# Optimization experiments

Hardware: AMD Instinct MI355X
Metric: run time of the kernel (lower is better)

## Reference

```python
import jax, jax.numpy as jnp
import numpy as np

EMBED_DIM = 128
SEQ_LEN = 2048
NUM_PHENOTYPES = 1
NUM_LAYERS = 3
INIT_SCALE = 0.03
BATCH = 32


def setup_inputs() -> dict:
    key = jax.random.key(0)
    ks = jax.random.split(key, 10)
    genotypes = jax.random.normal(ks[0], (BATCH, SEQ_LEN), dtype=jnp.float32)
    emb = INIT_SCALE * jax.random.normal(ks[1], (SEQ_LEN, EMBED_DIM), dtype=jnp.float32)
    # torch Linear weights are (out, in); stacked over layers
    qw = INIT_SCALE * jax.random.normal(ks[2], (NUM_LAYERS, EMBED_DIM, EMBED_DIM), dtype=jnp.float32)
    kw = INIT_SCALE * jax.random.normal(ks[3], (NUM_LAYERS, EMBED_DIM, EMBED_DIM), dtype=jnp.float32)
    vw = INIT_SCALE * jax.random.normal(ks[4], (NUM_LAYERS, EMBED_DIM, EMBED_DIM), dtype=jnp.float32)
    qb = jnp.zeros((NUM_LAYERS, EMBED_DIM), dtype=jnp.float32)
    kb = jnp.zeros((NUM_LAYERS, EMBED_DIM), dtype=jnp.float32)
    vb = jnp.zeros((NUM_LAYERS, EMBED_DIM), dtype=jnp.float32)
    bound = 1.0 / np.sqrt(SEQ_LEN * EMBED_DIM)
    rw = jax.random.uniform(ks[5], (NUM_PHENOTYPES, SEQ_LEN * EMBED_DIM), dtype=jnp.float32, minval=-bound, maxval=bound)
    rb = jax.random.uniform(ks[6], (NUM_PHENOTYPES,), dtype=jnp.float32, minval=-bound, maxval=bound)
    return {"genotypes": genotypes, "emb": emb, "qw": qw, "qb": qb,
            "kw": kw, "kb": kb, "vw": vw, "vb": vb, "rw": rw, "rb": rb}


def reference(genotypes, emb, qw, qb, kw, kb, vw, vb, rw, rb):
    # x: (B, L, D) = genotype value scales locus embedding
    x = genotypes[:, :, None] * emb[None, :, :]
    for i in range(NUM_LAYERS):
        # torch Linear: y = x @ W.T + b
        q = jnp.einsum('bld,ed->ble', x, qw[i]) + qb[i]
        k = jnp.einsum('bld,ed->ble', x, kw[i]) + kb[i]
        v = jnp.einsum('bld,ed->ble', x, vw[i]) + vb[i]
        scores = jnp.einsum('bqd,bkd->bqk', q, k)  # (B, L, L), unscaled
        attn = jax.nn.softmax(scores, axis=-1)
        x = jnp.einsum('bqk,bkd->bqd', attn, v)  # no skip connections
    x_flat = x.reshape(x.shape[0], -1)  # (B, L*D)
    return x_flat @ rw.T + rb  # (B, num_phenotypes)
```

## Files before the change

kernel.cpp:

```cpp
#include <hip/hip_runtime.h>
#include <hip/hip_bf16.h>

#define B_   32
#define L_   2048
#define D_   128
#define NL_  3
#define KVB  64
#define NKT  (L_ / KVB)

typedef __attribute__((ext_vector_type(8))) short short8;
typedef __attribute__((ext_vector_type(4))) float f32x4;
typedef __attribute__((ext_vector_type(16))) float f32x16;

__device__ __forceinline__ short f2bf(float f) {
    unsigned u = __builtin_bit_cast(unsigned, f);
    u += 0x7fffu + ((u >> 16) & 1u);
    return (short)(u >> 16);
}
__device__ __forceinline__ unsigned pk2(float a, float b) {
    unsigned ua = __builtin_bit_cast(unsigned, a);
    ua += 0x7fffu + ((ua >> 16) & 1u);
    unsigned ub = __builtin_bit_cast(unsigned, b);
    ub += 0x7fffu + ((ub >> 16) & 1u);
    return (ua >> 16) | (ub & 0xffff0000u);
}
__device__ __forceinline__ void plswap(unsigned& a, unsigned& b) {
    asm volatile("v_permlane32_swap_b32 %0, %1" : "+v"(a), "+v"(b));
}

__device__ __forceinline__ void gll16(const void* g, void* l) {
    __builtin_amdgcn_global_load_lds(
        (__attribute__((address_space(1))) void*)(g),
        (__attribute__((address_space(3))) void*)(l), 16, 0, 0);
}


__global__ __launch_bounds__(256) void k_form_x(const float* __restrict__ g,
                                                const float* __restrict__ emb,
                                                short* __restrict__ X) {
    int tid = blockIdx.x * 256 + threadIdx.x;
    int bl  = tid >> 4;
    int d8  = (tid & 15) << 3;
    int l   = bl & (L_ - 1);
    float gv = g[bl];
    const float4* e = reinterpret_cast<const float4*>(emb + (size_t)l * D_ + d8);
    float4 a = e[0], b = e[1];
    short8 r;
    r[0]=f2bf(a.x*gv); r[1]=f2bf(a.y*gv); r[2]=f2bf(a.z*gv); r[3]=f2bf(a.w*gv);
    r[4]=f2bf(b.x*gv); r[5]=f2bf(b.y*gv); r[6]=f2bf(b.z*gv); r[7]=f2bf(b.w*gv);
    *reinterpret_cast<short8*>(X + (size_t)tid * 8) = r;
}

__global__ __launch_bounds__(256) void k_convw(const float* __restrict__ qw,
                                               const float* __restrict__ kw,
                                               const float* __restrict__ vw,
                                               short* __restrict__ Wbf) {
    const float* src = (blockIdx.y == 0) ? qw : (blockIdx.y == 1) ? kw : vw;
    int tid = blockIdx.x * 256 + threadIdx.x;
    int layer = tid >> 11;
    int i = tid & 2047;
    int Lb = i * 16;
    int row = Lb >> 8, c = (Lb & 255) ^ ((row & 7) << 4);
    const float4* p = reinterpret_cast<const float4*>(src + (size_t)layer * 16384 + row * 128 + (c >> 1));
    float4 a = p[0], b = p[1];
    short8 s;
    s[0]=f2bf(a.x); s[1]=f2bf(a.y); s[2]=f2bf(a.z); s[3]=f2bf(a.w);
    s[4]=f2bf(b.x); s[5]=f2bf(b.y); s[6]=f2bf(b.z); s[7]=f2bf(b.w);
    size_t off = ((size_t)layer * 3 + blockIdx.y) * 16384;
    *reinterpret_cast<short8*>(Wbf + off + (size_t)i * 8) = s;
}

__global__ __launch_bounds__(256, 2) void k_qkv(const short* __restrict__ X,
    const short* __restrict__ Wl,
    const float* __restrict__ bq, const float* __restrict__ bk, const float* __restrict__ bv,
    short* __restrict__ Qf, short* __restrict__ Kf, short* __restrict__ Vf) {
    __shared__ short xs[128 * 128];
    __shared__ short wsh[128 * 128];
    const int t = threadIdx.x;
    int flat = blockIdx.x, xcd = flat & 7, idx = flat >> 3;
    int mat = idx >> 6, rblk = xcd * 64 + (idx & 63);
    const float* bias = (mat == 0) ? bq : (mat == 1) ? bk : bv;
    const short* Wg = Wl + (size_t)mat * 16384;
    const size_t rowbase = (size_t)rblk * 128;

    const char* Xg = reinterpret_cast<const char*>(X) + rowbase * 256;
#pragma unroll
    for (int p = 0; p < 8; p++) {
        int Lb = (p * 256 + t) * 16;
        int row = Lb >> 8, c = Lb & 255;
        gll16(Xg + (size_t)row * 256 + (c ^ ((row & 7) << 4)),
              reinterpret_cast<char*>(xs) + Lb);
    }
#pragma unroll
    for (int p = 0; p < 8; p++) {
        int Lb = (p * 256 + t) * 16;
        gll16(reinterpret_cast<const char*>(Wg) + Lb,
              reinterpret_cast<char*>(wsh) + Lb);
    }
    __syncthreads();

    const int wave = t >> 6, lane = t & 63, g = lane >> 4, ln = lane & 15;
    const int bb2 = (int)(rowbase >> 11);
    const int l0  = (int)(rowbase & (L_ - 1));
    f32x4 acc[2][8];
#pragma unroll
    for (int mi = 0; mi < 2; mi++)
#pragma unroll
        for (int ni = 0; ni < 8; ni++) acc[mi][ni] = f32x4{0.f, 0.f, 0.f, 0.f};

    if (mat < 2) {
#pragma unroll
        for (int kk = 0; kk < 4; kk++) {
            short8 aW[2];
#pragma unroll
            for (int mi = 0; mi < 2; mi++) {
                int row = wave * 32 + mi * 16 + ln;
                int byte = (row * 256 + kk * 64 + g * 16) ^ ((row & 7) << 4);
                aW[mi] = *reinterpret_cast<const short8*>(reinterpret_cast<const char*>(wsh) + byte);
            }
#pragma unroll
            for (int ni = 0; ni < 8; ni++) {
                int row = ni * 16 + ln;
                int byte = (row * 256 + kk * 64 + g * 16) ^ ((row & 7) << 4);
                short8 bX = *reinterpret_cast<const short8*>(reinterpret_cast<const char*>(xs) + byte);
                acc[0][ni] = __builtin_amdgcn_mfma_f32_16x16x32_bf16(aW[0], bX, acc[0][ni], 0, 0, 0);
                acc[1][ni] = __builtin_amdgcn_mfma_f32_16x16x32_bf16(aW[1], bX, acc[1][ni], 0, 0, 0);
            }
        }
        char* oc = reinterpret_cast<char*>((mat == 0) ? Qf : Kf) + ((size_t)bb2 << 19);
        int lidx_hi = ((g >> 1) & 1) << 5;
#pragma unroll
        for (int mi = 0; mi < 2; mi++) {
            int e0 = wave * 32 + mi * 16 + g * 4;
            int dst = wave * 2 + mi;
            float4 b4 = *reinterpret_cast<const float4*>(bias + e0);
#pragma unroll
            for (int ni = 0; ni < 8; ni++) {
                unsigned lo = (unsigned short)f2bf(acc[mi][ni][0] + b4.x)
                            | ((unsigned)(unsigned short)f2bf(acc[mi][ni][1] + b4.y) << 16);
                unsigned hi2 = (unsigned short)f2bf(acc[mi][ni][2] + b4.z)
                            | ((unsigned)(unsigned short)f2bf(acc[mi][ni][3] + b4.w) << 16);
                int blk32 = (l0 >> 5) + (ni >> 1);
                int l31 = ((ni & 1) << 4) + ln;
                size_t off = ((size_t)(blk32 * 8 + dst) << 10)
                           + ((lidx_hi + l31) << 4) + ((g & 1) << 3);
                int2 pk; pk.x = (int)lo; pk.y = (int)hi2;
                *reinterpret_cast<int2*>(oc + off) = pk;
            }
        }
    } else {
#pragma unroll
        for (int kk = 0; kk < 4; kk++) {
            short8 aX[2];
#pragma unroll
            for (int mi = 0; mi < 2; mi++) {
                int row = wave * 32 + mi * 16 + ln;
                int byte = (row * 256 + kk * 64 + g * 16) ^ ((row & 7) << 4);
                aX[mi] = *reinterpret_cast<const short8*>(reinterpret_cast<const char*>(xs) + byte);
            }
#pragma unroll
            for (int ni = 0; ni < 8; ni++) {
                int row = ni * 16 + ln;
                int byte = (row * 256 + kk * 64 + g * 16) ^ ((row & 7) << 4);
                short8 bW = *reinterpret_cast<const short8*>(reinterpret_cast<const char*>(wsh) + byte);
                acc[0][ni] = __builtin_amdgcn_mfma_f32_16x16x32_bf16(aX[0], bW, acc[0][ni], 0, 0, 0);
                acc[1][ni] = __builtin_amdgcn_mfma_f32_16x16x32_bf16(aX[1], bW, acc[1][ni], 0, 0, 0);
            }
        }
        char* oc = reinterpret_cast<char*>(Vf) + ((size_t)bb2 << 19);
#pragma unroll
        for (int ni = 0; ni < 8; ni++) {
            int d = ni * 16 + ln;
            float bvv = bias[d];
            int d2 = d >> 5, d31 = d & 31;
#pragma unroll
            for (int mi = 0; mi < 2; mi++) {
                unsigned lo = (unsigned short)f2bf(acc[mi][ni][0] + bvv)
                            | ((unsigned)(unsigned short)f2bf(acc[mi][ni][1] + bvv) << 16);
                unsigned hi2 = (unsigned short)f2bf(acc[mi][ni][2] + bvv)
                            | ((unsigned)(unsigned short)f2bf(acc[mi][ni][3] + bvv) << 16);
                int lglob = l0 + wave * 32 + mi * 16 + g * 4;
                int kt = lglob >> 6, k16 = (lglob >> 4) & 3, lhi = (lglob >> 3) & 1;
                size_t off = ((size_t)kt << 14) + (k16 << 12) + (d2 << 10)
                           + ((lhi * 32 + d31) << 4) + ((g & 1) << 3);
                int2 pk; pk.x = (int)lo; pk.y = (int)hi2;
                *reinterpret_cast<int2*>(oc + off) = pk;
            }
        }
    }
}

__global__ __launch_bounds__(256, 3) void k_attn(const short* __restrict__ Qf,
                                                 const short* __restrict__ Kf,
                                                 const short* __restrict__ Vf,
                                                 short* __restrict__ Xo,
                                                 const float* __restrict__ rw,
                                                 const float* __restrict__ rb,
                                                 float* __restrict__ out,
                                                 int fuse) {
    __shared__ short Ks[2][KVB * 128];
    __shared__ short Vts[128 * KVB];
    const int t = threadIdx.x, w = t >> 6, lane = t & 63;
    const int hi = lane >> 5, c5 = lane & 31;
    int flat = blockIdx.x;
    int xcd = flat & 7, idx = flat >> 3;
    int b = xcd * 4 + (idx >> 4), qt = idx & 15;
    const size_t qbase = (size_t)b * L_ + qt * 128;

    const char* Qg = reinterpret_cast<const char*>(Qf) + ((size_t)b << 19);
    short8 qf[8];
#pragma unroll
    for (int dst = 0; dst < 8; dst++)
        qf[dst] = *reinterpret_cast<const short8*>(
            Qg + (((size_t)(qt * 4 + w) * 8 + dst) << 10) + lane * 16);
    __builtin_amdgcn_sched_barrier(0);

    const char* Kg = reinterpret_cast<const char*>(Kf) + ((size_t)b << 19);
    const char* Vg = reinterpret_cast<const char*>(Vf) + ((size_t)b << 19);

    auto stageK = [&](int kt, int buf) {
#pragma unroll
        for (int p = 0; p < 4; p++) {
            int Lb = (p * 256 + t) * 16;
            gll16(Kg + ((size_t)kt << 14) + Lb, reinterpret_cast<char*>(Ks[buf]) + Lb);
        }
    };
    auto stageV = [&](int kt) {
#pragma unroll
        for (int p = 0; p < 4; p++) {
            int Lb = (p * 256 + t) * 16;
            gll16(Vg + ((size_t)kt << 14) + Lb, reinterpret_cast<char*>(Vts) + Lb);
        }
    };

    stageK(0, 0);
    stageV(0);
    stageK(1, 1);

    f32x16 o[4];
#pragma unroll
    for (int d2 = 0; d2 < 4; d2++)
#pragma unroll
        for (int r = 0; r < 16; r++) o[d2][r] = 0.f;
    float lsum = 0.f;

    for (int kt = 0; kt < NKT; kt++) {
        if (kt < NKT - 1) asm volatile("s_waitcnt vmcnt(4)" ::: "memory");
        else              asm volatile("s_waitcnt vmcnt(0)" ::: "memory");
        __builtin_amdgcn_sched_barrier(0);
        __builtin_amdgcn_s_barrier();

        const char* Kb8 = reinterpret_cast<const char*>(Ks[kt & 1]) + lane * 16;
        const char* Vb8 = reinterpret_cast<const char*>(Vts) + lane * 16;

        f32x16 s0, s1;
#pragma unroll
        for (int r = 0; r < 16; r++) { s0[r] = 0.f; s1[r] = 0.f; }
        __builtin_amdgcn_s_setprio(1);
#pragma unroll
        for (int dst = 0; dst < 8; dst++) {
            short8 kf0 = *reinterpret_cast<const short8*>(Kb8 + dst * 1024);
            short8 kf1 = *reinterpret_cast<const short8*>(Kb8 + 8192 + dst * 1024);
            s0 = __builtin_amdgcn_mfma_f32_32x32x16_bf16(kf0, qf[dst], s0, 0, 0, 0);
            s1 = __builtin_amdgcn_mfma_f32_32x32x16_bf16(kf1, qf[dst], s1, 0, 0, 0);
        }
        __builtin_amdgcn_s_setprio(0);

        float e0[16], e1[16];
#pragma unroll
        for (int r = 0; r < 16; r++) { e0[r] = __expf(s0[r]); e1[r] = __expf(s1[r]); }
#pragma unroll
        for (int r = 0; r < 16; r++) lsum += e0[r] + e1[r];

        short8 pa[4];
#pragma unroll
        for (int kt16 = 0; kt16 < 4; kt16++) {
            const float* e = (kt16 < 2) ? e0 : e1;
            int rb2 = (kt16 & 1) * 8;
            unsigned w01 = pk2(e[rb2 + 0], e[rb2 + 1]);
            unsigned w23 = pk2(e[rb2 + 2], e[rb2 + 3]);
            unsigned w45 = pk2(e[rb2 + 4], e[rb2 + 5]);
            unsigned w67 = pk2(e[rb2 + 6], e[rb2 + 7]);
            plswap(w01, w45);
            plswap(w23, w67);
            uint4 fr; fr.x = w01; fr.y = w23; fr.z = w45; fr.w = w67;
            pa[kt16] = __builtin_bit_cast(short8, fr);
        }

        __builtin_amdgcn_s_setprio(1);
#pragma unroll
        for (int kt16 = 0; kt16 < 4; kt16++) {
#pragma unroll
            for (int d2 = 0; d2 < 4; d2++) {
                short8 vf = *reinterpret_cast<const short8*>(Vb8 + kt16 * 4096 + d2 * 1024);
                o[d2] = __builtin_amdgcn_mfma_f32_32x32x16_bf16(pa[kt16], vf, o[d2], 0, 0, 0);
            }
        }
        __builtin_amdgcn_s_setprio(0);

        __builtin_amdgcn_sched_barrier(0);
        __builtin_amdgcn_s_barrier();
        if (kt + 1 < NKT) stageV(kt + 1);
        if (kt + 2 < NKT) stageK(kt + 2, kt & 1);
    }

    lsum += __shfl_xor(lsum, 32, 64);

    if (!fuse) {
#pragma unroll
        for (int reg = 0; reg < 16; reg++) {
            int crow = (reg & 3) + 8 * (reg >> 2) + 4 * hi;
            float inv = 1.0f / __shfl(lsum, crow, 64);
            size_t rowg = qbase + w * 32 + crow;
#pragma unroll
            for (int d2 = 0; d2 < 4; d2++)
                Xo[rowg * D_ + d2 * 32 + c5] = f2bf(o[d2][reg] * inv);
        }
    } else {
        float part = 0.f;
#pragma unroll
        for (int reg = 0; reg < 16; reg++) {
            int crow = (reg & 3) + 8 * (reg >> 2) + 4 * hi;
            float inv = 1.0f / __shfl(lsum, crow, 64);
            size_t rowg = (size_t)(qt * 128 + w * 32 + crow) * D_;
#pragma unroll
            for (int d2 = 0; d2 < 4; d2++)
                part += (o[d2][reg] * inv) * rw[rowg + d2 * 32 + c5];
        }
#pragma unroll
        for (int off = 32; off > 0; off >>= 1) part += __shfl_xor(part, off, 64);
        if (lane == 0) atomicAdd(out + b, part);
        if (qt == 0 && t == 0) atomicAdd(out + b, rb[0]);
    }
}

extern "C" void kernel_launch(void* const* d_in, const int* in_sizes, int n_in,
                              void* d_out, int out_size, void* d_ws, size_t ws_size,
                              hipStream_t stream) {
    const float* genotypes = (const float*)d_in[0];
    const float* emb       = (const float*)d_in[1];
    const float* qw        = (const float*)d_in[2];
    const float* qb        = (const float*)d_in[3];
    const float* kw        = (const float*)d_in[4];
    const float* kb        = (const float*)d_in[5];
    const float* vw        = (const float*)d_in[6];
    const float* vb        = (const float*)d_in[7];
    const float* rw        = (const float*)d_in[8];
    const float* rb        = (const float*)d_in[9];
    float* out = (float*)d_out;

    const size_t NBL = (size_t)B_ * L_;
    short* X   = (short*)d_ws;
    short* Qf  = X  + NBL * D_;
    short* Kf  = Qf + NBL * D_;
    short* Vf  = Kf + NBL * D_;
    short* Wbf = Vf + NBL * D_;

    hipMemsetAsync(out, 0, out_size * sizeof(float), stream);
    k_form_x<<<dim3((NBL * D_ / 8) / 256), 256, 0, stream>>>(genotypes, emb, X);
    k_convw<<<dim3(24, 3), 256, 0, stream>>>(qw, kw, vw, Wbf);
    for (int layer = 0; layer < NL_; layer++) {
        int boff = layer * D_;
        k_qkv<<<dim3(1536), 256, 0, stream>>>(X, Wbf + (size_t)layer * 3 * 16384,
                                              qb + boff, kb + boff, vb + boff,
                                              Qf, Kf, Vf);
        k_attn<<<dim3(512), 256, 0, stream>>>(Qf, Kf, Vf, X, rw, rb, out,
                                              layer == NL_ - 1 ? 1 : 0);
    }
}
```

Measured before the change: 354.3 us.

## Software-pipeline QK and PV across KV tiles with triple-buffered V and exp2 softmax

Restructures the attention loop so the QK^T MFMAs for tile kt are issued alongside the PV MFMAs for tile kt-1, with softmax placed after both, letting matrix and vector work overlap. V staging goes to a triple buffer and both K and V are prefetched two tiles ahead. Q is pre-scaled by log2(e) in the projection kernel so softmax can use raw v_exp_f32, and bf16 packing uses v_cvt_pk_bf16_f32 in place of manual rounding. Occupancy is lowered from 3 to 2 blocks per CU in launch bounds to fit the larger LDS and register footprint.

```diff
diff --git a/kernel.cpp b/kernel.cpp
--- a/kernel.cpp
+++ b/kernel.cpp
@@ -17,12 +17,11 @@
     u += 0x7fffu + ((u >> 16) & 1u);
     return (short)(u >> 16);
 }
-__device__ __forceinline__ unsigned pk2(float a, float b) {
-    unsigned ua = __builtin_bit_cast(unsigned, a);
-    ua += 0x7fffu + ((ua >> 16) & 1u);
-    unsigned ub = __builtin_bit_cast(unsigned, b);
-    ub += 0x7fffu + ((ub >> 16) & 1u);
-    return (ua >> 16) | (ub & 0xffff0000u);
+__device__ __forceinline__ float exp2g(float x) {
+    float r; asm("v_exp_f32 %0, %1" : "=v"(r) : "v"(x)); return r;
+}
+__device__ __forceinline__ unsigned cvtpk(float a, float b) {
+    unsigned r; asm("v_cvt_pk_bf16_f32 %0, %1, %2" : "=v"(r) : "v"(a), "v"(b)); return r;
 }
 __device__ __forceinline__ void plswap(unsigned& a, unsigned& b) {
     asm volatile("v_permlane32_swap_b32 %0, %1" : "+v"(a), "+v"(b));
@@ -127,6 +126,7 @@
                 acc[1][ni] = __builtin_amdgcn_mfma_f32_16x16x32_bf16(aW[1], bX, acc[1][ni], 0, 0, 0);
             }
         }
+        const float qscale = (mat == 0) ? 1.4426950408889634f : 1.0f;
         char* oc = reinterpret_cast<char*>((mat == 0) ? Qf : Kf) + ((size_t)bb2 << 19);
         int lidx_hi = ((g >> 1) & 1) << 5;
 #pragma unroll
@@ -136,10 +136,10 @@
             float4 b4 = *reinterpret_cast<const float4*>(bias + e0);
 #pragma unroll
             for (int ni = 0; ni < 8; ni++) {
-                unsigned lo = (unsigned short)f2bf(acc[mi][ni][0] + b4.x)
-                            | ((unsigned)(unsigned short)f2bf(acc[mi][ni][1] + b4.y) << 16);
-                unsigned hi2 = (unsigned short)f2bf(acc[mi][ni][2] + b4.z)
-                            | ((unsigned)(unsigned short)f2bf(acc[mi][ni][3] + b4.w) << 16);
+                unsigned lo = (unsigned short)f2bf((acc[mi][ni][0] + b4.x) * qscale)
+                            | ((unsigned)(unsigned short)f2bf((acc[mi][ni][1] + b4.y) * qscale) << 16);
+                unsigned hi2 = (unsigned short)f2bf((acc[mi][ni][2] + b4.z) * qscale)
+                            | ((unsigned)(unsigned short)f2bf((acc[mi][ni][3] + b4.w) * qscale) << 16);
                 int blk32 = (l0 >> 5) + (ni >> 1);
                 int l31 = ((ni & 1) << 4) + ln;
                 size_t off = ((size_t)(blk32 * 8 + dst) << 10)
@@ -190,7 +190,7 @@
     }
 }
 
-__global__ __launch_bounds__(256, 3) void k_attn(const short* __restrict__ Qf,
+__global__ __launch_bounds__(256, 2) void k_attn(const short* __restrict__ Qf,
                                                  const short* __restrict__ Kf,
                                                  const short* __restrict__ Vf,
                                                  short* __restrict__ Xo,
@@ -199,7 +199,7 @@
                                                  float* __restrict__ out,
                                                  int fuse) {
     __shared__ short Ks[2][KVB * 128];
-    __shared__ short Vts[128 * KVB];
+    __shared__ short Vts[3][128 * KVB];
     const int t = threadIdx.x, w = t >> 6, lane = t & 63;
     const int hi = lane >> 5, c5 = lane & 31;
     int flat = blockIdx.x;
@@ -218,24 +218,22 @@
     const char* Kg = reinterpret_cast<const char*>(Kf) + ((size_t)b << 19);
     const char* Vg = reinterpret_cast<const char*>(Vf) + ((size_t)b << 19);
 
-    auto stageK = [&](int kt, int buf) {
+    auto stageK = [&](int kt) {
 #pragma unroll
         for (int p = 0; p < 4; p++) {
             int Lb = (p * 256 + t) * 16;
-            gll16(Kg + ((size_t)kt << 14) + Lb, reinterpret_cast<char*>(Ks[buf]) + Lb);
+            gll16(Kg + ((size_t)kt << 14) + Lb, reinterpret_cast<char*>(Ks[kt & 1]) + Lb);
         }
     };
     auto stageV = [&](int kt) {
 #pragma unroll
         for (int p = 0; p < 4; p++) {
             int Lb = (p * 256 + t) * 16;
-            gll16(Vg + ((size_t)kt << 14) + Lb, reinterpret_cast<char*>(Vts) + Lb);
-        }
-    };
-
-    stageK(0, 0);
-    stageV(0);
-    stageK(1, 1);
+            gll16(Vg + ((size_t)kt << 14) + Lb, reinterpret_cast<char*>(Vts[kt % 3]) + Lb);
+        }
+    };
+
+    stageK(0); stageV(0); stageK(1); stageV(1);
 
     f32x16 o[4];
 #pragma unroll
@@ -243,17 +241,30 @@
 #pragma unroll
         for (int r = 0; r < 16; r++) o[d2][r] = 0.f;
     float lsum = 0.f;
-
-    for (int kt = 0; kt < NKT; kt++) {
-        if (kt < NKT - 1) asm volatile("s_waitcnt vmcnt(4)" ::: "memory");
-        else              asm volatile("s_waitcnt vmcnt(0)" ::: "memory");
-        __builtin_amdgcn_sched_barrier(0);
-        __builtin_amdgcn_s_barrier();
-
+    short8 pa[4];
+
+    auto softmax = [&](const f32x16& s0, const f32x16& s1) {
+        float e0[16], e1[16];
+#pragma unroll
+        for (int r = 0; r < 16; r++) { e0[r] = exp2g(s0[r]); e1[r] = exp2g(s1[r]); }
+#pragma unroll
+        for (int r = 0; r < 16; r++) lsum += e0[r] + e1[r];
+#pragma unroll
+        for (int kt16 = 0; kt16 < 4; kt16++) {
+            const float* e = (kt16 < 2) ? e0 : e1;
+            int rb2 = (kt16 & 1) * 8;
+            unsigned w01 = cvtpk(e[rb2 + 0], e[rb2 + 1]);
+            unsigned w23 = cvtpk(e[rb2 + 2], e[rb2 + 3]);
+            unsigned w45 = cvtpk(e[rb2 + 4], e[rb2 + 5]);
+            unsigned w67 = cvtpk(e[rb2 + 6], e[rb2 + 7]);
+            plswap(w01, w45);
+            plswap(w23, w67);
+            uint4 fr; fr.x = w01; fr.y = w23; fr.z = w45; fr.w = w67;
+            pa[kt16] = __builtin_bit_cast(short8, fr);
+        }
+    };
+    auto qk = [&](int kt, f32x16& s0, f32x16& s1) {
         const char* Kb8 = reinterpret_cast<const char*>(Ks[kt & 1]) + lane * 16;
-        const char* Vb8 = reinterpret_cast<const char*>(Vts) + lane * 16;
-
-        f32x16 s0, s1;
 #pragma unroll
         for (int r = 0; r < 16; r++) { s0[r] = 0.f; s1[r] = 0.f; }
         __builtin_amdgcn_s_setprio(1);
@@ -265,28 +276,9 @@
             s1 = __builtin_amdgcn_mfma_f32_32x32x16_bf16(kf1, qf[dst], s1, 0, 0, 0);
         }
         __builtin_amdgcn_s_setprio(0);
-
-        float e0[16], e1[16];
-#pragma unroll
-        for (int r = 0; r < 16; r++) { e0[r] = __expf(s0[r]); e1[r] = __expf(s1[r]); }
-#pragma unroll
-        for (int r = 0; r < 16; r++) lsum += e0[r] + e1[r];
-
-        short8 pa[4];
-#pragma unroll
-        for (int kt16 = 0; kt16 < 4; kt16++) {
-            const float* e = (kt16 < 2) ? e0 : e1;
-            int rb2 = (kt16 & 1) * 8;
-            unsigned w01 = pk2(e[rb2 + 0], e[rb2 + 1]);
-            unsigned w23 = pk2(e[rb2 + 2], e[rb2 + 3]);
-            unsigned w45 = pk2(e[rb2 + 4], e[rb2 + 5]);
-            unsigned w67 = pk2(e[rb2 + 6], e[rb2 + 7]);
-            plswap(w01, w45);
-            plswap(w23, w67);
-            uint4 fr; fr.x = w01; fr.y = w23; fr.z = w45; fr.w = w67;
-            pa[kt16] = __builtin_bit_cast(short8, fr);
-        }
-
+    };
+    auto pv = [&](int kt) {
+        const char* Vb8 = reinterpret_cast<const char*>(Vts[kt % 3]) + lane * 16;
         __builtin_amdgcn_s_setprio(1);
 #pragma unroll
         for (int kt16 = 0; kt16 < 4; kt16++) {
@@ -297,12 +289,33 @@
             }
         }
         __builtin_amdgcn_s_setprio(0);
-
+    };
+
+    {
+        asm volatile("s_waitcnt vmcnt(8)" ::: "memory");
         __builtin_amdgcn_sched_barrier(0);
         __builtin_amdgcn_s_barrier();
-        if (kt + 1 < NKT) stageV(kt + 1);
-        if (kt + 2 < NKT) stageK(kt + 2, kt & 1);
-    }
+        f32x16 s0, s1;
+        qk(0, s0, s1);
+        softmax(s0, s1);
+        __builtin_amdgcn_sched_barrier(0);
+        __builtin_amdgcn_s_barrier();
+        stageV(2); stageK(2);
+    }
+    for (int kt = 1; kt < NKT; kt++) {
+        if (kt < NKT - 1) asm volatile("s_waitcnt vmcnt(8)" ::: "memory");
+        else              asm volatile("s_waitcnt vmcnt(0)" ::: "memory");
+        __builtin_amdgcn_sched_barrier(0);
+        __builtin_amdgcn_s_barrier();
+        f32x16 s0, s1;
+        qk(kt, s0, s1);
+        pv(kt - 1);
+        softmax(s0, s1);
+        __builtin_amdgcn_sched_barrier(0);
+        __builtin_amdgcn_s_barrier();
+        if (kt + 2 < NKT) { stageV(kt + 2); stageK(kt + 2); }
+    }
+    pv(NKT - 1);
 
     lsum += __shfl_xor(lsum, 32, 64);
 
```

After: 339.0 us. -4.3%, faster.
